# Kernel optimization log

Measured on AMD Instinct MI355X. Metric: run time of the kernel, lower is better.

The kernel has to match this reference:

```python
import jax, jax.numpy as jnp
import numpy as np

NPOINT = 2048
NSAMPLE = 32
BN_EPS = 1e-5


def fps(xyz_t, npoint):
    """Furthest point sampling. xyz_t: [B,N,3] -> idx [B,npoint] (starts at index 0)."""
    B, N, _ = xyz_t.shape

    def step(carry, _):
        dist, last = carry  # dist [B,N], last [B]
        centroid = jnp.take_along_axis(xyz_t, last[:, None, None], axis=1)  # [B,1,3]
        d = jnp.sum((xyz_t - centroid) ** 2, axis=-1)  # [B,N]
        dist = jnp.minimum(dist, d)
        nxt = jnp.argmax(dist, axis=1).astype(jnp.int32)
        return (dist, nxt), last

    init = (jnp.full((B, N), 1e10, xyz_t.dtype), jnp.zeros((B,), jnp.int32))
    _, idx = jax.lax.scan(step, init, None, length=npoint)  # [npoint,B]
    return jnp.transpose(idx)  # [B,npoint]


def knn(k, query_t, ref_t):
    """query_t [B,S,3], ref_t [B,N,3] -> k-nearest indices [B,S,k]."""
    d = (jnp.sum(query_t ** 2, -1)[:, :, None]
         + jnp.sum(ref_t ** 2, -1)[:, None, :]
         - 2.0 * jnp.einsum('bsc,bnc->bsn', query_t, ref_t))  # [B,S,N]
    _, idx = jax.lax.top_k(-d, k)
    return idx


def group(feat_t, idx):
    """feat_t [B,N,C], idx [B,S,K] -> [B,S,K,C] gathered neighbors."""
    return jax.vmap(lambda f, i: f[i])(feat_t, idx)


def setup_inputs():
    key = jax.random.key(0)
    ks = jax.random.split(key, 8)
    B, N, C, D = 8, 8192, 3, 3
    mlp = [32, 32, 64]
    inp = {
        'xyz': jax.random.normal(ks[0], (B, C, N), jnp.float32),
        'points': jax.random.normal(ks[1], (B, D, N), jnp.float32),
    }
    last = D + 3  # conv input channels = in_channel + 3
    for i, oc in enumerate(mlp):
        inp[f'w{i}'] = jax.random.normal(ks[2 + i], (oc, last), jnp.float32) * (1.0 / np.sqrt(last))
        inp[f'g{i}'] = jnp.ones((oc,), jnp.float32)
        inp[f'b{i}'] = jnp.zeros((oc,), jnp.float32)
        last = oc
    return inp


def reference(xyz, points, w0, g0, b0, w1, g1, b1, w2, g2, b2):
    xyz_t = jnp.transpose(xyz, (0, 2, 1))        # [B,N,3]
    points_t = jnp.transpose(points, (0, 2, 1))  # [B,N,D]

    fps_idx = fps(xyz_t, NPOINT)                             # [B,S]
    new_xyz_t = jax.vmap(lambda f, i: f[i])(xyz_t, fps_idx)  # [B,S,3]

    knn_idx = knn(NSAMPLE, new_xyz_t, xyz_t)                 # [B,S,K]
    grouped_xyz = group(xyz_t, knn_idx)                      # [B,S,K,3]
    pos_diff = grouped_xyz - new_xyz_t[:, :, None, :]        # [B,S,K,3]
    grouped_pts = group(points_t, knn_idx)                   # [B,S,K,D]

    x = jnp.concatenate([pos_diff, grouped_pts], axis=-1)    # [B,S,K,3+D]
    for w, g, b in ((w0, g0, b0), (w1, g1, b1), (w2, g2, b2)):
        x = jnp.einsum('oc,bskc->bsko', w, x)                # 1x1 conv, no bias
        mean = jnp.mean(x, axis=(0, 1, 2))                   # BatchNorm2d (training stats)
        var = jnp.var(x, axis=(0, 1, 2))
        x = jax.nn.relu(g * (x - mean) * jax.lax.rsqrt(var + BN_EPS) + b)

    new_points = jnp.max(x, axis=2)  # max over K neighbors -> [B,S,C']
    new_xyz = jnp.transpose(new_xyz_t, (0, 2, 1))      # [B,3,S]
    new_points = jnp.transpose(new_points, (0, 2, 1))  # [B,C',S]
    return (new_xyz, new_points, fps_idx)
```

## Files before the change

### kernel.cpp

```cpp
#include <hip/hip_runtime.h>
#include <hip/hip_bf16.h>
#include <math.h>


#define NB 8
#define NN 8192
#define NS 2048
#define NK 32

typedef float f32x2 __attribute__((ext_vector_type(2)));

__global__ __launch_bounds__(256) void prep_kernel(const float* __restrict__ xyz,
                                                   const float* __restrict__ pts,
                                                   float4* __restrict__ xyz4,
                                                   float4* __restrict__ pts4) {
  int g = blockIdx.x * 256 + threadIdx.x;
  int b = g >> 13, n = g & 8191;
  const float* xb = xyz + b * 3 * NN;
  float x = xb[n], y = xb[NN + n], z = xb[2 * NN + n];
  xyz4[g] = make_float4(x, y, z, fmaf(x, x, fmaf(y, y, z * z)));
  const float* pb = pts + b * 3 * NN;
  pts4[g] = make_float4(pb[n], pb[NN + n], pb[2 * NN + n], 0.f);
}

template <int CTRL>
__device__ __forceinline__ float dpp_max(float v) {
  int o = __builtin_amdgcn_update_dpp(__float_as_int(v), __float_as_int(v),
                                      CTRL, 0xf, 0xf, false);
  return fmaxf(v, __int_as_float(o));
}
__device__ __forceinline__ void barrier_lgkm() {
  asm volatile("s_waitcnt lgkmcnt(0)\n\ts_barrier" ::: "memory");
}

__global__ __launch_bounds__(512, 1) void fps_kernel(const float4* __restrict__ xyz4,
                                                     float* __restrict__ out_nxyz,
                                                     float* __restrict__ out_fps,
                                                     float4* __restrict__ nxyz4) {
#pragma clang fp contract(off)
  int b = blockIdx.x, tid = threadIdx.x;
  int lane = tid & 63, wid = tid >> 6;
  __shared__ float4 tbl[NN];
  __shared__ unsigned long long kslot[2][8];
  const float4* xb = xyz4 + b * NN;

  f32x2 px[8], py[8], pz[8], dist[8];
#pragma unroll
  for (int jj = 0; jj < 8; ++jj) {
    float4 t0 = xb[(tid << 4) + 2 * jj];
    float4 t1 = xb[(tid << 4) + 2 * jj + 1];
    tbl[(tid << 4) + 2 * jj] = t0;
    tbl[(tid << 4) + 2 * jj + 1] = t1;
    px[jj] = (f32x2){t0.x, t1.x};
    py[jj] = (f32x2){t0.y, t1.y};
    pz[jj] = (f32x2){t0.z, t1.z};
    dist[jj] = (f32x2){1e10f, 1e10f};
  }

  float4 c0 = xb[0];
  float cx = c0.x, cy = c0.y, cz = c0.z;
  float* onx = out_nxyz + b * 3 * NS;
  if (tid == 0) {
    nxyz4[b * NS] = c0;
    onx[0] = c0.x;
    onx[NS] = c0.y;
    onx[2 * NS] = c0.z;
    out_fps[b * NS] = 0.f;
  }

  for (int s = 1; s < NS; ++s) {
    f32x2 c2x = {cx, cx}, c2y = {cy, cy}, c2z = {cz, cz};
#pragma unroll
    for (int jj = 0; jj < 8; ++jj) {
      f32x2 dx = px[jj] - c2x;
      f32x2 dy = py[jj] - c2y;
      f32x2 dz = pz[jj] - c2z;
      f32x2 d = (dx * dx + dy * dy) + dz * dz;
      f32x2 dm;
      dm[0] = fminf(dist[jj][0], d[0]);
      dm[1] = fminf(dist[jj][1], d[1]);
      dist[jj] = dm;
    }
    f32x2 m2 = dist[0];
#pragma unroll
    for (int jj = 1; jj < 8; ++jj) {
      m2[0] = fmaxf(m2[0], dist[jj][0]);
      m2[1] = fmaxf(m2[1], dist[jj][1]);
    }
    float best = fmaxf(m2[0], m2[1]);
    int bj = 0;
#pragma unroll
    for (int j = 15; j >= 0; --j)
      bj = (dist[j >> 1][j & 1] == best) ? j : bj;

    float mm = best;
    mm = dpp_max<0x111>(mm);
    mm = dpp_max<0x112>(mm);
    mm = dpp_max<0x114>(mm);
    mm = dpp_max<0x118>(mm);
    mm = dpp_max<0x142>(mm);
    mm = dpp_max<0x143>(mm);
    float wmax = __int_as_float(__builtin_amdgcn_readlane(__float_as_int(mm), 63));

    unsigned long long bl = __ballot(best == wmax);
    int l0 = __ffsll(bl) - 1;
    int gw = __builtin_amdgcn_readlane((tid << 4) + bj, l0);

    if (lane == 0)
      kslot[s & 1][wid] = (((unsigned long long)__float_as_uint(wmax)) << 32) |
                          (unsigned)(8191 - gw);
    barrier_lgkm();

    const ulonglong2* kv = (const ulonglong2*)kslot[s & 1];
    ulonglong2 q0 = kv[0], q1 = kv[1], q2 = kv[2], q3 = kv[3];
    unsigned long long a0 = q0.x > q0.y ? q0.x : q0.y;
    unsigned long long a1 = q1.x > q1.y ? q1.x : q1.y;
    unsigned long long a2 = q2.x > q2.y ? q2.x : q2.y;
    unsigned long long a3 = q3.x > q3.y ? q3.x : q3.y;
    unsigned long long b0 = a0 > a1 ? a0 : a1;
    unsigned long long b1 = a2 > a3 ? a2 : a3;
    unsigned long long km = b0 > b1 ? b0 : b1;
    int gid = 8191 - (int)((unsigned)km & 0x1FFFu);
    gid = __builtin_amdgcn_readfirstlane(gid);

    float4 c = tbl[gid];
    cx = c.x; cy = c.y; cz = c.z;
    if (tid == 0) {
      nxyz4[b * NS + s] = c;
      onx[s] = c.x;
      onx[NS + s] = c.y;
      onx[2 * NS + s] = c.z;
      out_fps[b * NS + s] = (float)gid;
    }
  }
}

__device__ __forceinline__ void insert32(float (&a)[32], float f) {
#pragma unroll
  for (int i = 31; i >= 1; --i) a[i] = fminf(a[i], fmaxf(a[i - 1], f));
  a[0] = fminf(a[0], f);
}

__global__ __launch_bounds__(256) void knn_kernel(const float4* __restrict__ xyz4,
                                                  const float4* __restrict__ nxyz4,
                                                  int* __restrict__ knn) {
  __shared__ float lbuf[256][33];
  int b = blockIdx.x >> 5, tile = blockIdx.x & 31;
  int tid = threadIdx.x;
  int q = tid & 63, chunk = tid >> 6;
  float4 Q = nxyz4[b * NS + tile * 64 + q];
  float qq = Q.w;
  float mx = -2.f * Q.x, my = -2.f * Q.y, mz = -2.f * Q.z;
  float arr[32];
#pragma unroll
  for (int i = 0; i < 32; ++i) arr[i] = __uint_as_float(0x7f7fffffu);

  const float4* refs = xyz4 + b * NN + chunk * 2048;
  int rbase = chunk * 2048;
  for (int r = 0; r < 2048; ++r) {
    float4 R = refs[r];
    float d = fmaf(R.x, mx, fmaf(R.y, my, fmaf(R.z, mz, R.w + qq)));
    d = fmaxf(d, 0.f);
    float f = __uint_as_float((__float_as_uint(d) & 0xFFFFE000u) | (unsigned)(rbase + r));
    if (f < arr[31]) insert32(arr, f);
  }
#pragma unroll
  for (int i = 0; i < 32; ++i) lbuf[tid][i] = arr[i];
  __syncthreads();
  if (tid < 64) {
    for (int c = 1; c < 4; ++c)
      for (int i = 0; i < 32; ++i) {
        float f = lbuf[c * 64 + tid][i];
        if (f < arr[31]) insert32(arr, f);
      }
    int base = (b * NS + tile * 64 + tid) * NK;
#pragma unroll
    for (int i = 0; i < 32; ++i) knn[base + i] = (int)(__float_as_uint(arr[i]) & 0x1FFFu);
  }
}

template <int STAGE>
__global__ __launch_bounds__(256) void mlp_kernel(
    const float4* __restrict__ xyz4, const float4* __restrict__ pts4,
    const float4* __restrict__ nxyz4, const int* __restrict__ knn,
    const float* __restrict__ w0, const float* __restrict__ w1,
    const float* __restrict__ w2, const float* __restrict__ ab,
    float* __restrict__ partials, float* __restrict__ out_np) {
  constexpr int C = (STAGE == 2) ? 64 : 32;
  constexpr int SM = (STAGE == 3) ? 8 * 64 * 32 : 512;
  __shared__ float smem[SM];
  int blk = blockIdx.x;
  int b = blk >> 6, s0 = (blk & 63) * 32;
  int tid = threadIdx.x, sl = tid & 31, ksec = tid >> 5;
  int lane = tid & 63, wid = tid >> 6;
  int s = s0 + sl;
  float4 Q = nxyz4[b * NS + s];
  const float4* xb = xyz4 + b * NN;
  const float4* pb = pts4 + b * NN;
  const int* kb = knn + (b * NS + s) * NK + ksec * 4;

  float acc1[(STAGE == 3) ? 64 : C];
  float acc2[(STAGE == 3) ? 1 : C];
  if constexpr (STAGE == 3) {
#pragma unroll
    for (int o = 0; o < 64; ++o) acc1[o] = -3.4e38f;
  } else {
#pragma unroll
    for (int o = 0; o < C; ++o) { acc1[o] = 0.f; acc2[o] = 0.f; }
  }

  for (int kk = 0; kk < 4; ++kk) {
    int nid = kb[kk];
    float4 R = xb[nid];
    float4 P = pb[nid];
    float x0[6] = {R.x - Q.x, R.y - Q.y, R.z - Q.z, P.x, P.y, P.z};
    float h[32];
#pragma unroll
    for (int o = 0; o < 32; ++o) {
      float a = w0[o * 6] * x0[0];
#pragma unroll
      for (int c = 1; c < 6; ++c) a = fmaf(w0[o * 6 + c], x0[c], a);
      h[o] = a;
    }
    if constexpr (STAGE == 0) {
#pragma unroll
      for (int o = 0; o < 32; ++o) { acc1[o] += h[o]; acc2[o] = fmaf(h[o], h[o], acc2[o]); }
    } else {
#pragma unroll
      for (int o = 0; o < 32; ++o) h[o] = fmaxf(fmaf(h[o], ab[o], ab[64 + o]), 0.f);
      float h1[32];
#pragma unroll
      for (int o = 0; o < 32; ++o) {
        float a = 0.f;
#pragma unroll
        for (int i = 0; i < 32; ++i) a = fmaf(w1[o * 32 + i], h[i], a);
        h1[o] = a;
      }
      if constexpr (STAGE == 1) {
#pragma unroll
        for (int o = 0; o < 32; ++o) { acc1[o] += h1[o]; acc2[o] = fmaf(h1[o], h1[o], acc2[o]); }
      } else {
#pragma unroll
        for (int o = 0; o < 32; ++o) h1[o] = fmaxf(fmaf(h1[o], ab[128 + o], ab[192 + o]), 0.f);
#pragma unroll
        for (int o = 0; o < 64; ++o) {
          float a = 0.f;
#pragma unroll
          for (int i = 0; i < 32; ++i) a = fmaf(w2[o * 32 + i], h1[i], a);
          if constexpr (STAGE == 2) {
            acc1[o] += a;
            acc2[o] = fmaf(a, a, acc2[o]);
          } else {
            acc1[o] = fmaxf(acc1[o], fmaxf(fmaf(a, ab[256 + o], ab[320 + o]), 0.f));
          }
        }
      }
    }
  }

  if constexpr (STAGE < 3) {
#pragma unroll
    for (int o = 0; o < C; ++o) {
      float v1 = acc1[o], v2 = acc2[o];
#pragma unroll
      for (int d = 1; d < 64; d <<= 1) { v1 += __shfl_xor(v1, d); v2 += __shfl_xor(v2, d); }
      acc1[o] = v1; acc2[o] = v2;
    }
    if (lane == 0) {
#pragma unroll
      for (int o = 0; o < C; ++o) {
        smem[wid * 2 * C + o] = acc1[o];
        smem[wid * 2 * C + C + o] = acc2[o];
      }
    }
    __syncthreads();
    if (tid < 2 * C) {
      float v = smem[tid] + smem[2 * C + tid] + smem[4 * C + tid] + smem[6 * C + tid];
      partials[tid * 512 + blk] = v;
    }
  } else {
#pragma unroll
    for (int o = 0; o < 64; ++o) smem[ksec * 2048 + o * 32 + sl] = acc1[o];
    __syncthreads();
#pragma unroll
    for (int i = 0; i < 8; ++i) {
      int e = i * 256 + tid;
      int ch = e >> 5, ss = e & 31;
      float v = smem[ch * 32 + ss];
#pragma unroll
      for (int ks = 1; ks < 8; ++ks) v = fmaxf(v, smem[ks * 2048 + ch * 32 + ss]);
      out_np[b * 64 * NS + ch * NS + s0 + ss] = v;
    }
  }
}

__global__ __launch_bounds__(256) void finalize_kernel(const float* __restrict__ partials,
                                                       const float* __restrict__ g,
                                                       const float* __restrict__ bt,
                                                       float* __restrict__ ab, int C) {
  __shared__ float sm[128];
  int tid = threadIdx.x, lane = tid & 63, wid = tid >> 6;
  for (int ch = wid; ch < 2 * C; ch += 4) {
    const float* p = partials + ch * 512;
    float acc = 0.f;
#pragma unroll
    for (int i = 0; i < 8; ++i) acc += p[i * 64 + lane];
#pragma unroll
    for (int d = 1; d < 64; d <<= 1) acc += __shfl_xor(acc, d);
    if (lane == 0) sm[ch] = acc;
  }
  __syncthreads();
  if (tid < C) {
    float s1 = sm[tid];
    float s2 = sm[C + tid];
    const float ninv = 1.0f / 524288.0f;
    float mean = s1 * ninv;
    float var = s2 * ninv - mean * mean;
    float inv = 1.0f / sqrtf(var + 1e-5f);
    float a = g[tid] * inv;
    ab[tid] = a;
    ab[64 + tid] = bt[tid] - mean * a;
  }
}

extern "C" void kernel_launch(void* const* d_in, const int* in_sizes, int n_in,
                              void* d_out, int out_size, void* d_ws, size_t ws_size,
                              hipStream_t stream) {
  const float* xyz = (const float*)d_in[0];
  const float* pts = (const float*)d_in[1];
  const float* w0 = (const float*)d_in[2];
  const float* g0 = (const float*)d_in[3];
  const float* b0 = (const float*)d_in[4];
  const float* w1 = (const float*)d_in[5];
  const float* g1 = (const float*)d_in[6];
  const float* b1 = (const float*)d_in[7];
  const float* w2 = (const float*)d_in[8];
  const float* g2 = (const float*)d_in[9];
  const float* b2 = (const float*)d_in[10];
  float* out = (float*)d_out;
  float* ws = (float*)d_ws;

  float4* xyz4 = (float4*)ws;
  float4* pts4 = (float4*)(ws + 262144);
  float4* nxyz4 = (float4*)(ws + 524288);
  int* knn = (int*)(ws + 589824);
  float* partials = ws + 1114112;
  float* ab = ws + 1310720;
  float* out_np = out + 49152;
  float* out_fps = out + 1097728;

  prep_kernel<<<256, 256, 0, stream>>>(xyz, pts, xyz4, pts4);
  fps_kernel<<<NB, 512, 0, stream>>>(xyz4, out, out_fps, nxyz4);
  knn_kernel<<<256, 256, 0, stream>>>(xyz4, nxyz4, knn);

  mlp_kernel<0><<<512, 256, 0, stream>>>(xyz4, pts4, nxyz4, knn, w0, w1, w2, ab, partials, nullptr);
  finalize_kernel<<<1, 256, 0, stream>>>(partials, g0, b0, ab, 32);
  mlp_kernel<1><<<512, 256, 0, stream>>>(xyz4, pts4, nxyz4, knn, w0, w1, w2, ab, partials + 65536, nullptr);
  finalize_kernel<<<1, 256, 0, stream>>>(partials + 65536, g1, b1, ab + 128, 32);
  mlp_kernel<2><<<512, 256, 0, stream>>>(xyz4, pts4, nxyz4, knn, w0, w1, w2, ab, partials + 131072, nullptr);
  finalize_kernel<<<1, 256, 0, stream>>>(partials + 131072, g2, b2, ab + 256, 64);
  mlp_kernel<3><<<512, 256, 0, stream>>>(xyz4, pts4, nxyz4, knn, w0, w1, w2, ab, nullptr, out_np);
}
```

Baseline: 3.291 ms.

## Fuse prep into FPS kernel, restrict argmax scan to winning lanes, transpose partials

Removes the separate prep kernel by having the FPS kernel read the raw planar xyz/points, build the float4 tables, and write them to global memory during its load phase. The per-iteration index search over 16 candidates now runs only in lanes whose local max equals the wave max, using a bitmask and ffs instead of a select chain on every lane. BatchNorm partials are stored block-major, and finalize sums them with one thread per channel over two halves instead of wave reductions. Trade-offs: the FPS prologue does strided planar loads from only 8 blocks, and the finalize loop is serial per thread.

```diff
diff --git a/kernel.cpp b/kernel.cpp
--- a/kernel.cpp
+++ b/kernel.cpp
@@ -9,19 +9,6 @@
 #define NK 32
 
 typedef float f32x2 __attribute__((ext_vector_type(2)));
-
-__global__ __launch_bounds__(256) void prep_kernel(const float* __restrict__ xyz,
-                                                   const float* __restrict__ pts,
-                                                   float4* __restrict__ xyz4,
-                                                   float4* __restrict__ pts4) {
-  int g = blockIdx.x * 256 + threadIdx.x;
-  int b = g >> 13, n = g & 8191;
-  const float* xb = xyz + b * 3 * NN;
-  float x = xb[n], y = xb[NN + n], z = xb[2 * NN + n];
-  xyz4[g] = make_float4(x, y, z, fmaf(x, x, fmaf(y, y, z * z)));
-  const float* pb = pts + b * 3 * NN;
-  pts4[g] = make_float4(pb[n], pb[NN + n], pb[2 * NN + n], 0.f);
-}
 
 template <int CTRL>
 __device__ __forceinline__ float dpp_max(float v) {
@@ -33,7 +20,10 @@
   asm volatile("s_waitcnt lgkmcnt(0)\n\ts_barrier" ::: "memory");
 }
 
-__global__ __launch_bounds__(512, 1) void fps_kernel(const float4* __restrict__ xyz4,
+__global__ __launch_bounds__(512, 1) void fps_kernel(const float* __restrict__ xyz,
+                                                     const float* __restrict__ pts,
+                                                     float4* __restrict__ xyz4,
+                                                     float4* __restrict__ pts4,
                                                      float* __restrict__ out_nxyz,
                                                      float* __restrict__ out_fps,
                                                      float4* __restrict__ nxyz4) {
@@ -42,29 +32,37 @@
   int lane = tid & 63, wid = tid >> 6;
   __shared__ float4 tbl[NN];
   __shared__ unsigned long long kslot[2][8];
-  const float4* xb = xyz4 + b * NN;
+  const float* xsrc = xyz + b * 3 * NN;
+  const float* psrc = pts + b * 3 * NN;
+  float4* xg = xyz4 + b * NN;
+  float4* pg = pts4 + b * NN;
 
   f32x2 px[8], py[8], pz[8], dist[8];
 #pragma unroll
   for (int jj = 0; jj < 8; ++jj) {
-    float4 t0 = xb[(tid << 4) + 2 * jj];
-    float4 t1 = xb[(tid << 4) + 2 * jj + 1];
-    tbl[(tid << 4) + 2 * jj] = t0;
-    tbl[(tid << 4) + 2 * jj + 1] = t1;
-    px[jj] = (f32x2){t0.x, t1.x};
-    py[jj] = (f32x2){t0.y, t1.y};
-    pz[jj] = (f32x2){t0.z, t1.z};
+    int n0 = (tid << 4) + 2 * jj, n1 = n0 + 1;
+    float x0 = xsrc[n0], y0 = xsrc[NN + n0], z0 = xsrc[2 * NN + n0];
+    float x1 = xsrc[n1], y1 = xsrc[NN + n1], z1 = xsrc[2 * NN + n1];
+    float4 t0 = make_float4(x0, y0, z0, fmaf(x0, x0, fmaf(y0, y0, z0 * z0)));
+    float4 t1 = make_float4(x1, y1, z1, fmaf(x1, x1, fmaf(y1, y1, z1 * z1)));
+    xg[n0] = t0; xg[n1] = t1;
+    tbl[n0] = t0; tbl[n1] = t1;
+    px[jj] = (f32x2){x0, x1};
+    py[jj] = (f32x2){y0, y1};
+    pz[jj] = (f32x2){z0, z1};
     dist[jj] = (f32x2){1e10f, 1e10f};
-  }
-
-  float4 c0 = xb[0];
-  float cx = c0.x, cy = c0.y, cz = c0.z;
+    pg[n0] = make_float4(psrc[n0], psrc[NN + n0], psrc[2 * NN + n0], 0.f);
+    pg[n1] = make_float4(psrc[n1], psrc[NN + n1], psrc[2 * NN + n1], 0.f);
+  }
+
+  float cx = xsrc[0], cy = xsrc[NN], cz = xsrc[2 * NN];
   float* onx = out_nxyz + b * 3 * NS;
   if (tid == 0) {
-    nxyz4[b * NS] = c0;
-    onx[0] = c0.x;
-    onx[NS] = c0.y;
-    onx[2 * NS] = c0.z;
+    nxyz4[b * NS] = make_float4(cx, cy, cz,
+                                fmaf(cx, cx, fmaf(cy, cy, cz * cz)));
+    onx[0] = cx;
+    onx[NS] = cy;
+    onx[2 * NS] = cz;
     out_fps[b * NS] = 0.f;
   }
 
@@ -88,10 +86,6 @@
       m2[1] = fmaxf(m2[1], dist[jj][1]);
     }
     float best = fmaxf(m2[0], m2[1]);
-    int bj = 0;
-#pragma unroll
-    for (int j = 15; j >= 0; --j)
-      bj = (dist[j >> 1][j & 1] == best) ? j : bj;
 
     float mm = best;
     mm = dpp_max<0x111>(mm);
@@ -104,7 +98,21 @@
 
     unsigned long long bl = __ballot(best == wmax);
     int l0 = __ffsll(bl) - 1;
-    int gw = __builtin_amdgcn_readlane((tid << 4) + bj, l0);
+
+    unsigned bj = 0;
+    if (best == wmax) {
+      unsigned t16[16];
+#pragma unroll
+      for (int j = 0; j < 16; ++j)
+        t16[j] = (dist[j >> 1][j & 1] == best) ? (1u << j) : 0u;
+#pragma unroll
+      for (int j = 0; j < 8; ++j) t16[j] |= t16[j + 8];
+#pragma unroll
+      for (int j = 0; j < 4; ++j) t16[j] |= t16[j + 4];
+      unsigned mask = (t16[0] | t16[2]) | (t16[1] | t16[3]);
+      bj = __ffs(mask) - 1;
+    }
+    int gw = __builtin_amdgcn_readlane((tid << 4) + (int)bj, l0);
 
     if (lane == 0)
       kslot[s & 1][wid] = (((unsigned long long)__float_as_uint(wmax)) << 32) |
@@ -276,7 +284,7 @@
     __syncthreads();
     if (tid < 2 * C) {
       float v = smem[tid] + smem[2 * C + tid] + smem[4 * C + tid] + smem[6 * C + tid];
-      partials[tid * 512 + blk] = v;
+      partials[blk * 128 + tid] = v;
     }
   } else {
 #pragma unroll
@@ -298,21 +306,19 @@
                                                        const float* __restrict__ g,
                                                        const float* __restrict__ bt,
                                                        float* __restrict__ ab, int C) {
-  __shared__ float sm[128];
-  int tid = threadIdx.x, lane = tid & 63, wid = tid >> 6;
-  for (int ch = wid; ch < 2 * C; ch += 4) {
-    const float* p = partials + ch * 512;
-    float acc = 0.f;
-#pragma unroll
-    for (int i = 0; i < 8; ++i) acc += p[i * 64 + lane];
-#pragma unroll
-    for (int d = 1; d < 64; d <<= 1) acc += __shfl_xor(acc, d);
-    if (lane == 0) sm[ch] = acc;
-  }
+  __shared__ float sm[256];
+  int tid = threadIdx.x;
+  int ch = tid & 127, half = tid >> 7;
+  float acc = 0.f;
+  if (ch < 2 * C) {
+    const float* p = partials + half * 256 * 128 + ch;
+    for (int i = 0; i < 256; ++i) acc += p[i * 128];
+  }
+  sm[half * 128 + ch] = acc;
   __syncthreads();
   if (tid < C) {
-    float s1 = sm[tid];
-    float s2 = sm[C + tid];
+    float s1 = sm[tid] + sm[128 + tid];
+    float s2 = sm[C + tid] + sm[128 + C + tid];
     const float ninv = 1.0f / 524288.0f;
     float mean = s1 * ninv;
     float var = s2 * ninv - mean * mean;
@@ -349,8 +355,7 @@
   float* out_np = out + 49152;
   float* out_fps = out + 1097728;
 
-  prep_kernel<<<256, 256, 0, stream>>>(xyz, pts, xyz4, pts4);
-  fps_kernel<<<NB, 512, 0, stream>>>(xyz4, out, out_fps, nxyz4);
+  fps_kernel<<<NB, 512, 0, stream>>>(xyz, pts, xyz4, pts4, out, out_fps, nxyz4);
   knn_kernel<<<256, 256, 0, stream>>>(xyz4, nxyz4, knn);
 
   mlp_kernel<0><<<512, 256, 0, stream>>>(xyz4, pts4, nxyz4, knn, w0, w1, w2, ab, partials, nullptr);
```

Measured after the change: 3.217 ms. 2.3% less time.
